# Kernel tuning notes

Hardware: AMD Instinct MI355X
Metric: run time of the kernel (lower is better)

The kernel has to match this reference:

```python
import jax, jax.numpy as jnp
import numpy as np

B, L, FUT = 500, 100, 4  # dialogs, utterances per dialog, to_future_link
N = B * L
IN, HID, NC = 1024, 512, 7


def _build_graph():
    # per-dialog local edges: node i -> i (self) and i -> i+1..i+FUT (within dialog)
    i = np.arange(L)[:, None]                       # [L,1]
    off = np.arange(FUT + 1)[None, :]               # [1,FUT+1]
    tgt_local = i + off                             # [L,FUT+1]
    valid = tgt_local < L
    src_local = np.broadcast_to(i, tgt_local.shape)[valid]
    tgt_local = tgt_local[valid]                    # [E_per]
    base = (np.arange(B) * L)[:, None]              # [B,1]
    src = (base + src_local[None, :]).reshape(-1)
    tgt = (base + tgt_local[None, :]).reshape(-1)
    edges = np.stack([src, tgt], axis=0).astype(np.int64)  # [2,E], E=245000
    rng = np.random.RandomState(0)
    speakers = rng.randint(0, 2, size=N).astype(np.int64)
    rel = (speakers[src] * speakers[tgt]).astype(np.int64)  # in {0,1}
    return edges, rel


def setup_inputs() -> dict:
    key = jax.random.key(0)
    ks = jax.random.split(key, 8)
    edges, rel = _build_graph()
    s = 0.02
    return {
        "x": jax.random.normal(ks[0], (N, IN), dtype=jnp.float32),
        "edges": jnp.asarray(edges),
        "relation_type": jnp.asarray(rel),
        "w_rel": jax.random.normal(ks[1], (2, IN, HID), dtype=jnp.float32) * s,
        "w_root": jax.random.normal(ks[2], (IN, HID), dtype=jnp.float32) * s,
        "b_rgcn": jnp.zeros((HID,), jnp.float32),
        "w_gc_rel": jax.random.normal(ks[3], (HID, HID), dtype=jnp.float32) * s,
        "w_gc_root": jax.random.normal(ks[4], (HID, HID), dtype=jnp.float32) * s,
        "b_gc": jnp.zeros((HID,), jnp.float32),
        "w_skip": jax.random.normal(ks[5], (IN, HID), dtype=jnp.float32) * s,
        "b_skip": jnp.zeros((HID,), jnp.float32),
        "w_clf": jax.random.normal(ks[6], (HID, NC), dtype=jnp.float32) * s,
        "b_clf": jnp.zeros((NC,), jnp.float32),
    }


def reference(x, edges, relation_type, w_rel, w_root, b_rgcn,
              w_gc_rel, w_gc_root, b_gc, w_skip, b_skip, w_clf, b_clf):
    n = x.shape[0]
    src, tgt = edges[0], edges[1]
    # --- RGCNConv(IN, HID, 2), aggr='mean' per relation, root weight + bias ---
    x_src = x[src]  # [E, IN] gather
    h = x @ w_root + b_rgcn
    for r in range(2):
        m = (relation_type == r).astype(x.dtype)                    # [E]
        s = jax.ops.segment_sum(x_src * m[:, None], tgt, num_segments=n)  # [N,IN]
        c = jax.ops.segment_sum(m, tgt, num_segments=n)             # [N]
        mean = s / jnp.maximum(c, 1.0)[:, None]                     # scatter-mean, 0 if empty
        h = h + mean @ w_rel[r]
    # --- GraphConv(HID, HID), aggr='add': W_rel * sum_j x_j + W_root * x_i + b ---
    agg = jax.ops.segment_sum(h[src], tgt, num_segments=n)          # [N,HID]
    h2 = agg @ w_gc_rel + b_gc + h @ w_gc_root
    # --- classify(h2 + skip(x)) ---
    out = (h2 + x @ w_skip + b_skip) @ w_clf + b_clf                # [N,NC]
    return out
```

## Files before the change

### kernel.cpp

```cpp
#include <hip/hip_runtime.h>


#define DIAG_L 100
#define EPERD  490
#define NC     7
#define NROWS  50000
#define NBLK   782

using u16 = unsigned short;
using u32 = unsigned int;
typedef __bf16 bf16x8 __attribute__((ext_vector_type(8)));
typedef float  f32x4  __attribute__((ext_vector_type(4)));

__device__ __forceinline__ u16 f2b(float f) {
  u32 u = __builtin_bit_cast(u32, f);
  u32 r = (u + 0x7FFFu + ((u >> 16) & 1u)) >> 16;
  return (u16)r;
}
__device__ __forceinline__ u32 pk2(float a, float b) {
  return (u32)f2b(a) | ((u32)f2b(b) << 16);
}

__device__ __forceinline__ int pre_edges(int s) {
  int d = s - 96;
  return 5 * s - (d > 0 ? ((d * (d + 1)) >> 1) : 0);
}

__global__ __launch_bounds__(64)
void k_t1n(const float* __restrict__ w_gc_root, const float* __restrict__ w_gc_rel,
           const float* __restrict__ w_clf, const float* __restrict__ b_gc,
           const float* __restrict__ b_skip, const float* __restrict__ b_clf,
           float* __restrict__ tbl, float* __restrict__ cvec) {
  const int bid = blockIdx.x, l = threadIdx.x;
  if (bid < 1024) {
    const int which = bid & 1, k = bid >> 1;
    const float* src = (which ? w_gc_rel : w_gc_root) + (size_t)k * 512;
    float p[7] = {0.f, 0.f, 0.f, 0.f, 0.f, 0.f, 0.f};
#pragma unroll
    for (int jj = 0; jj < 8; ++jj) {
      int j = jj * 64 + l;
      float sv = src[j];
      const float* wc = w_clf + (size_t)j * 7;
#pragma unroll
      for (int c = 0; c < 7; ++c) p[c] += sv * wc[c];
    }
#pragma unroll
    for (int c = 0; c < 7; ++c)
      for (int d = 32; d; d >>= 1) p[c] += __shfl_xor(p[c], d);
    if (l == 0) {
      float* tr = tbl + which * 4096 + k * 8;
#pragma unroll
      for (int c = 0; c < 7; ++c) tr[c] = p[c];
      tr[7] = 0.f;
    }
  } else {
    const int c = bid - 1024;
    float s = 0.f;
#pragma unroll
    for (int jj = 0; jj < 8; ++jj) {
      int j = jj * 64 + l;
      s += (b_gc[j] + b_skip[j]) * w_clf[(size_t)j * 7 + c];
    }
    for (int d = 32; d; d >>= 1) s += __shfl_xor(s, d);
    if (l == 0) cvec[16 + c] = s + b_clf[c];
  }
}

__global__ __launch_bounds__(256)
void k_w64n(const float* __restrict__ w_root, const float* __restrict__ w_rel,
            const float* __restrict__ w_skip, const float* __restrict__ w_clf,
            const float* __restrict__ b_rgcn, const float* __restrict__ tbl,
            u16* __restrict__ BT, float* __restrict__ cvec) {
  const int bid = blockIdx.x;
  if (bid < 1024) {
    const int k = bid, tid = threadIdx.x;
    const int n = tid >> 2, jq = tid & 3, g = n >> 3, c = n & 7;
    float p = 0.f;
    if (g < 7 && c < 7) {
      const float* src;
      switch (g % 3) {
        case 0: src = w_root; break;
        case 1: src = w_rel; break;
        default: src = w_rel + 524288; break;
      }
      if (g == 6) src = w_skip;
      src += (size_t)k * 512;
      if (g == 6) {
#pragma unroll 4
        for (int i = 0; i < 128; ++i) {
          int j = jq * 128 + i;
          p += src[j] * w_clf[(size_t)j * 7 + c];
        }
      } else {
        const float* T = tbl + (g >= 3 ? 4096 : 0);
#pragma unroll 4
        for (int i = 0; i < 128; ++i) {
          int j = jq * 128 + i;
          p += src[j] * T[j * 8 + c];
        }
      }
    }
    p += __shfl_xor(p, 1); p += __shfl_xor(p, 2);
    if (jq == 0) BT[(size_t)n * 1024 + k] = f2b(p);
  } else {
    const int idx = bid - 1024;
    const int l = threadIdx.x;
    if (l < 64) {
      const float* T = tbl + (idx >= 8 ? 4096 : 0);
      const int cc = idx & 7;
      float s = 0.f;
#pragma unroll
      for (int jj = 0; jj < 8; ++jj) {
        int j = jj * 64 + l;
        s += b_rgcn[j] * T[j * 8 + cc];
      }
      for (int d = 32; d; d >>= 1) s += __shfl_xor(s, d);
      if (l == 0) cvec[idx] = s;
    }
  }
}

__device__ __forceinline__ void gload16(const void* g, void* l) {
  __builtin_amdgcn_global_load_lds(
      (const __attribute__((address_space(1))) u32*)g,
      (__attribute__((address_space(3))) u32*)l, 16, 0, 0);
}

__global__ __launch_bounds__(256, 5)
void k_px3(const float* __restrict__ x, const u16* __restrict__ BT,
           float* __restrict__ P) {
  __shared__ char lds[32768];
  const int tid = threadIdx.x;
  const int w = tid >> 6, l = tid & 63;
  const int rl = l & 15, sl = l >> 4;
  const int rb = blockIdx.x << 6;
  const int sx = (rl & 7) << 4;

  const int ar = tid >> 2, ac4 = tid & 3;
  int arow = rb + ar; if (arow > NROWS - 1) arow = NROWS - 1;
  const char* axp = (const char*)x + (size_t)arow * 4096 + ac4 * 64;
  const int aw0 = ar * 128 + ((ac4 * 32) ^ ((ar & 7) << 4));
  const int aw1 = ar * 128 + ((ac4 * 32 + 16) ^ ((ar & 7) << 4));

  const char* bsrc[2]; int blbase[2];
#pragma unroll
  for (int is = 0; is < 2; ++is) {
    int ci = is * 256 + tid;
    int r = ci >> 3, g = ci & 7, gp = g ^ (r & 7);
    bsrc[is] = (const char*)BT + (size_t)r * 2048 + gp * 16;
    blbase[is] = __builtin_amdgcn_readfirstlane(16384 + is * 4096 + w * 1024);
  }

  float4 av[4];
#define ALOAD(kt) { av[0] = *(const float4*)(axp + (kt) * 256);      \
                    av[1] = *(const float4*)(axp + (kt) * 256 + 16); \
                    av[2] = *(const float4*)(axp + (kt) * 256 + 32); \
                    av[3] = *(const float4*)(axp + (kt) * 256 + 48); }
#define AWRITE(bf) { uint4 q0, q1;                                   \
    q0.x = pk2(av[0].x, av[0].y); q0.y = pk2(av[0].z, av[0].w);      \
    q0.z = pk2(av[1].x, av[1].y); q0.w = pk2(av[1].z, av[1].w);      \
    q1.x = pk2(av[2].x, av[2].y); q1.y = pk2(av[2].z, av[2].w);      \
    q1.z = pk2(av[3].x, av[3].y); q1.w = pk2(av[3].z, av[3].w);      \
    *(uint4*)(lds + (bf) * 8192 + aw0) = q0;                         \
    *(uint4*)(lds + (bf) * 8192 + aw1) = q1; }
#define BSTAGE(bf, kt) {                                             \
    gload16(bsrc[0] + (kt) * 128, lds + blbase[0] + (bf) * 8192);    \
    gload16(bsrc[1] + (kt) * 128, lds + blbase[1] + (bf) * 8192); }

  f32x4 acc[4];
#pragma unroll
  for (int nf = 0; nf < 4; ++nf) acc[nf] = f32x4{0.f, 0.f, 0.f, 0.f};

  ALOAD(0); BSTAGE(0, 0); AWRITE(0);
  ALOAD(1); BSTAGE(1, 1); AWRITE(1);
  asm volatile("s_waitcnt lgkmcnt(0)" ::: "memory");
  __builtin_amdgcn_s_barrier();

  for (int t = 0; t < 16; ++t) {
    const int b = t & 1;
    const char* Ab = lds + b * 8192 + (w * 16 + rl) * 128;
    const char* Bb = lds + 16384 + b * 8192 + rl * 128;
    const int kn = (t + 2 < 16) ? t + 2 : 15;
    ALOAD(kn);
#pragma unroll
    for (int ks = 0; ks < 2; ++ks) {
      const int ko = (ks * 64 + sl * 16) ^ sx;
      bf16x8 af = *(const bf16x8*)(Ab + ko);
      bf16x8 b0 = *(const bf16x8*)(Bb + ko);
      bf16x8 b1 = *(const bf16x8*)(Bb + 2048 + ko);
      bf16x8 b2 = *(const bf16x8*)(Bb + 4096 + ko);
      bf16x8 b3 = *(const bf16x8*)(Bb + 6144 + ko);
      acc[0] = __builtin_amdgcn_mfma_f32_16x16x32_bf16(af, b0, acc[0], 0, 0, 0);
      acc[1] = __builtin_amdgcn_mfma_f32_16x16x32_bf16(af, b1, acc[1], 0, 0, 0);
      acc[2] = __builtin_amdgcn_mfma_f32_16x16x32_bf16(af, b2, acc[2], 0, 0, 0);
      acc[3] = __builtin_amdgcn_mfma_f32_16x16x32_bf16(af, b3, acc[3], 0, 0, 0);
    }
    __builtin_amdgcn_s_barrier();
    BSTAGE(b, kn);
    AWRITE(b);
    asm volatile("s_waitcnt lgkmcnt(0)" ::: "memory");
    __builtin_amdgcn_s_barrier();
  }
  asm volatile("s_waitcnt vmcnt(0)" ::: "memory");
#undef ALOAD
#undef AWRITE
#undef BSTAGE

  const int pr = rb + w * 16 + sl * 4;
#pragma unroll
  for (int nf = 0; nf < 4; ++nf)
#pragma unroll
    for (int j = 0; j < 4; ++j)
      P[(size_t)(pr + j) * 64 + nf * 16 + rl] = acc[nf][j];
}

__global__ __launch_bounds__(128)
void k_out(const float* __restrict__ P, const int* __restrict__ rel,
           const float* __restrict__ cvec, float* __restrict__ out) {
  __shared__ float pt[64 * 100 + 16 * 100];
  float* hb = pt + 6400;
  const int d = blockIdx.x;
  const int tid = threadIdx.x;
  const float* Pd = P + (size_t)d * DIAG_L * 64;

  for (int it = tid; it < 6400; it += 128) {
    int r = it >> 6, c = it & 63;
    pt[c * 100 + r] = Pd[it];
  }
  __syncthreads();

  const int ebase = d * EPERD;
  if (tid < DIAG_L) {
    const int u = tid;
    const int slo = (u > 4) ? u - 4 : 0;
    float S0A[7], S1A[7], S0B[7], S1B[7];
#pragma unroll
    for (int c = 0; c < 7; ++c) { S0A[c] = 0.f; S1A[c] = 0.f; S0B[c] = 0.f; S1B[c] = 0.f; }
    float c0 = 0.f, c1 = 0.f;
    for (int s = slo; s <= u; ++s) {
      int r = rel[ebase + pre_edges(s) + (u - s)];
      float m0 = r ? 0.f : 1.f, m1 = 1.f - m0;
      c0 += m0; c1 += m1;
#pragma unroll
      for (int c = 0; c < 7; ++c) {
        S0A[c] += m0 * pt[(8 + c)  * 100 + s];
        S1A[c] += m1 * pt[(16 + c) * 100 + s];
        S0B[c] += m0 * pt[(32 + c) * 100 + s];
        S1B[c] += m1 * pt[(40 + c) * 100 + s];
      }
    }
    float inv0 = 1.f / fmaxf(c0, 1.f), inv1 = 1.f / fmaxf(c1, 1.f);
#pragma unroll
    for (int c = 0; c < 7; ++c) {
      hb[c * 100 + u]       = pt[c * 100 + u]        + cvec[c]     + inv0 * S0A[c] + inv1 * S1A[c];
      hb[(8 + c) * 100 + u] = pt[(24 + c) * 100 + u] + cvec[8 + c] + inv0 * S0B[c] + inv1 * S1B[c];
    }
  }
  __syncthreads();

  if (tid < DIAG_L) {
    const int t = tid;
    const int slo = (t > 4) ? t - 4 : 0;
    float o[7];
#pragma unroll
    for (int c = 0; c < 7; ++c)
      o[c] = hb[c * 100 + t] + pt[(48 + c) * 100 + t] + cvec[16 + c];
    for (int s = slo; s <= t; ++s) {
#pragma unroll
      for (int c = 0; c < 7; ++c) o[c] += hb[(8 + c) * 100 + s];
    }
    float* op = out + ((size_t)d * DIAG_L + t) * NC;
#pragma unroll
    for (int c = 0; c < 7; ++c) op[c] = o[c];
  }
}

extern "C" void kernel_launch(void* const* d_in, const int* in_sizes, int n_in,
                              void* d_out, int out_size, void* d_ws, size_t ws_size,
                              hipStream_t stream) {
  const float* x         = (const float*)d_in[0];
  const int*   rel       = (const int*)d_in[2];
  const float* w_rel     = (const float*)d_in[3];
  const float* w_root    = (const float*)d_in[4];
  const float* b_rgcn    = (const float*)d_in[5];
  const float* w_gc_rel  = (const float*)d_in[6];
  const float* w_gc_root = (const float*)d_in[7];
  const float* b_gc      = (const float*)d_in[8];
  const float* w_skip    = (const float*)d_in[9];
  const float* b_skip    = (const float*)d_in[10];
  const float* w_clf     = (const float*)d_in[11];
  const float* b_clf     = (const float*)d_in[12];
  float* out = (float*)d_out;

  char* ws = (char*)d_ws;
  float* P    = (float*)(ws);
  u16*   BT   = (u16*)(ws + 12845056);
  float* tbl  = (float*)(ws + 12976128);
  float* cvec = (float*)(ws + 13008896);

  k_t1n<<<1031, 64, 0, stream>>>(w_gc_root, w_gc_rel, w_clf, b_gc, b_skip, b_clf, tbl, cvec);
  k_w64n<<<1040, 256, 0, stream>>>(w_root, w_rel, w_skip, w_clf, b_rgcn, tbl, BT, cvec);
  k_px3<<<NBLK, 256, 0, stream>>>(x, BT, P);
  k_out<<<500, 128, 0, stream>>>(P, rel, cvec, out);
}
```

Baseline: 82.12 us.

## Fuse projection GEMM with graph aggregation and classifier output using halo rows

Merges the bf16 MFMA projection kernel and the per-dialog aggregation/output kernel into one kernel. Each workgroup now computes 80 projected rows: its own 64 plus a 16-row halo of earlier rows, with wave 0 doing the extra MFMA tile. The results stay in LDS, and the RGCN mean, GraphConv sum and output are computed there directly, removing the global write and re-read of the intermediate P buffer and one kernel launch. It also remaps block IDs in an XCD-aware way. In exchange it recomputes the halo rows, loads wave 0 more heavily than the others, and enlarges LDS, lowering the occupancy target from 5 to 4.

Result: slower. 84.06 us (+2.4%).

```diff
diff --git a/kernel.cpp b/kernel.cpp
--- a/kernel.cpp
+++ b/kernel.cpp
@@ -126,50 +126,83 @@
       (__attribute__((address_space(3))) u32*)l, 16, 0, 0);
 }
 
-__global__ __launch_bounds__(256, 5)
-void k_px3(const float* __restrict__ x, const u16* __restrict__ BT,
-           float* __restrict__ P) {
-  __shared__ char lds[32768];
+__global__ __launch_bounds__(256, 4)
+void k_pxo(const float* __restrict__ x, const u16* __restrict__ BT,
+           const int* __restrict__ rel, const float* __restrict__ cvec,
+           float* __restrict__ out, int nwg) {
+  __shared__ char lds[36864];
   const int tid = threadIdx.x;
   const int w = tid >> 6, l = tid & 63;
   const int rl = l & 15, sl = l >> 4;
-  const int rb = blockIdx.x << 6;
   const int sx = (rl & 7) << 4;
 
-  const int ar = tid >> 2, ac4 = tid & 3;
-  int arow = rb + ar; if (arow > NROWS - 1) arow = NROWS - 1;
-  const char* axp = (const char*)x + (size_t)arow * 4096 + ac4 * 64;
-  const int aw0 = ar * 128 + ((ac4 * 32) ^ ((ar & 7) << 4));
-  const int aw1 = ar * 128 + ((ac4 * 32 + 16) ^ ((ar & 7) << 4));
+  const int bid = blockIdx.x;
+  const int q = nwg >> 3, r8 = nwg & 7;
+  const int xcd = bid & 7, bix = bid >> 3;
+  const int wg = (xcd < r8 ? xcd * (q + 1) : r8 * (q + 1) + (xcd - r8) * q) + bix;
+  const int gbase = wg * 64 - 16;
+
+  const bool dual = (tid < 64);
+  const int r0c = tid >> 2, s0c = tid & 3;
+  int g0r = gbase + r0c;
+  g0r = g0r < 0 ? 0 : (g0r > NROWS - 1 ? NROWS - 1 : g0r);
+  const char* axp0 = (const char*)x + (size_t)g0r * 4096 + s0c * 64;
+  const int a00 = r0c * 128 + ((s0c * 32) ^ ((r0c & 7) << 4));
+  const int a01 = r0c * 128 + ((s0c * 32 + 16) ^ ((r0c & 7) << 4));
+  const int r1c = 64 + (tid >> 2);
+  int g1r = gbase + r1c;
+  g1r = g1r < 0 ? 0 : (g1r > NROWS - 1 ? NROWS - 1 : g1r);
+  const char* axp1 = (const char*)x + (size_t)g1r * 4096 + s0c * 64;
+  const int a10 = r1c * 128 + ((s0c * 32) ^ ((r1c & 7) << 4));
+  const int a11 = r1c * 128 + ((s0c * 32 + 16) ^ ((r1c & 7) << 4));
 
   const char* bsrc[2]; int blbase[2];
 #pragma unroll
   for (int is = 0; is < 2; ++is) {
     int ci = is * 256 + tid;
-    int r = ci >> 3, g = ci & 7, gp = g ^ (r & 7);
-    bsrc[is] = (const char*)BT + (size_t)r * 2048 + gp * 16;
-    blbase[is] = __builtin_amdgcn_readfirstlane(16384 + is * 4096 + w * 1024);
-  }
-
-  float4 av[4];
-#define ALOAD(kt) { av[0] = *(const float4*)(axp + (kt) * 256);      \
-                    av[1] = *(const float4*)(axp + (kt) * 256 + 16); \
-                    av[2] = *(const float4*)(axp + (kt) * 256 + 32); \
-                    av[3] = *(const float4*)(axp + (kt) * 256 + 48); }
-#define AWRITE(bf) { uint4 q0, q1;                                   \
-    q0.x = pk2(av[0].x, av[0].y); q0.y = pk2(av[0].z, av[0].w);      \
-    q0.z = pk2(av[1].x, av[1].y); q0.w = pk2(av[1].z, av[1].w);      \
-    q1.x = pk2(av[2].x, av[2].y); q1.y = pk2(av[2].z, av[2].w);      \
-    q1.z = pk2(av[3].x, av[3].y); q1.w = pk2(av[3].z, av[3].w);      \
-    *(uint4*)(lds + (bf) * 8192 + aw0) = q0;                         \
-    *(uint4*)(lds + (bf) * 8192 + aw1) = q1; }
-#define BSTAGE(bf, kt) {                                             \
-    gload16(bsrc[0] + (kt) * 128, lds + blbase[0] + (bf) * 8192);    \
+    int rB = ci >> 3, gB = ci & 7, gp = gB ^ (rB & 7);
+    bsrc[is] = (const char*)BT + (size_t)rB * 2048 + gp * 16;
+    blbase[is] = __builtin_amdgcn_readfirstlane(20480 + is * 4096 + w * 1024);
+  }
+
+  float4 av0[4], av1[4];
+
+#define ALOAD(kt) { \
+    av0[0] = *(const float4*)(axp0 + (kt) * 256);        \
+    av0[1] = *(const float4*)(axp0 + (kt) * 256 + 16);   \
+    av0[2] = *(const float4*)(axp0 + (kt) * 256 + 32);   \
+    av0[3] = *(const float4*)(axp0 + (kt) * 256 + 48);   \
+    if (dual) {                                          \
+      av1[0] = *(const float4*)(axp1 + (kt) * 256);      \
+      av1[1] = *(const float4*)(axp1 + (kt) * 256 + 16); \
+      av1[2] = *(const float4*)(axp1 + (kt) * 256 + 32); \
+      av1[3] = *(const float4*)(axp1 + (kt) * 256 + 48); \
+    } }
+#define AWRITE(bf) { uint4 q0, q1;                              \
+    q0.x = pk2(av0[0].x, av0[0].y); q0.y = pk2(av0[0].z, av0[0].w); \
+    q0.z = pk2(av0[1].x, av0[1].y); q0.w = pk2(av0[1].z, av0[1].w); \
+    q1.x = pk2(av0[2].x, av0[2].y); q1.y = pk2(av0[2].z, av0[2].w); \
+    q1.z = pk2(av0[3].x, av0[3].y); q1.w = pk2(av0[3].z, av0[3].w); \
+    *(uint4*)(lds + (bf) * 10240 + a00) = q0;                   \
+    *(uint4*)(lds + (bf) * 10240 + a01) = q1;                   \
+    if (dual) { uint4 q2, q3;                                   \
+      q2.x = pk2(av1[0].x, av1[0].y); q2.y = pk2(av1[0].z, av1[0].w); \
+      q2.z = pk2(av1[1].x, av1[1].y); q2.w = pk2(av1[1].z, av1[1].w); \
+      q3.x = pk2(av1[2].x, av1[2].y); q3.y = pk2(av1[2].z, av1[2].w); \
+      q3.z = pk2(av1[3].x, av1[3].y); q3.w = pk2(av1[3].z, av1[3].w); \
+      *(uint4*)(lds + (bf) * 10240 + a10) = q2;                 \
+      *(uint4*)(lds + (bf) * 10240 + a11) = q3;                 \
+    } }
+#define BSTAGE(bf, kt) {                                            \
+    gload16(bsrc[0] + (kt) * 128, lds + blbase[0] + (bf) * 8192);   \
     gload16(bsrc[1] + (kt) * 128, lds + blbase[1] + (bf) * 8192); }
 
-  f32x4 acc[4];
-#pragma unroll
-  for (int nf = 0; nf < 4; ++nf) acc[nf] = f32x4{0.f, 0.f, 0.f, 0.f};
+  f32x4 acc[4], acc4[4];
+#pragma unroll
+  for (int nf = 0; nf < 4; ++nf) {
+    acc[nf]  = f32x4{0.f, 0.f, 0.f, 0.f};
+    acc4[nf] = f32x4{0.f, 0.f, 0.f, 0.f};
+  }
 
   ALOAD(0); BSTAGE(0, 0); AWRITE(0);
   ALOAD(1); BSTAGE(1, 1); AWRITE(1);
@@ -178,10 +211,11 @@
 
   for (int t = 0; t < 16; ++t) {
     const int b = t & 1;
-    const char* Ab = lds + b * 8192 + (w * 16 + rl) * 128;
-    const char* Bb = lds + 16384 + b * 8192 + rl * 128;
     const int kn = (t + 2 < 16) ? t + 2 : 15;
     ALOAD(kn);
+    const char* Ab  = lds + b * 10240 + (w * 16 + rl) * 128;
+    const char* Ab4 = lds + b * 10240 + (64 + rl) * 128;
+    const char* Bb  = lds + 20480 + b * 8192 + rl * 128;
 #pragma unroll
     for (int ks = 0; ks < 2; ++ks) {
       const int ko = (ks * 64 + sl * 16) ^ sx;
@@ -194,6 +228,13 @@
       acc[1] = __builtin_amdgcn_mfma_f32_16x16x32_bf16(af, b1, acc[1], 0, 0, 0);
       acc[2] = __builtin_amdgcn_mfma_f32_16x16x32_bf16(af, b2, acc[2], 0, 0, 0);
       acc[3] = __builtin_amdgcn_mfma_f32_16x16x32_bf16(af, b3, acc[3], 0, 0, 0);
+      if (w == 0) {
+        bf16x8 af4 = *(const bf16x8*)(Ab4 + ko);
+        acc4[0] = __builtin_amdgcn_mfma_f32_16x16x32_bf16(af4, b0, acc4[0], 0, 0, 0);
+        acc4[1] = __builtin_amdgcn_mfma_f32_16x16x32_bf16(af4, b1, acc4[1], 0, 0, 0);
+        acc4[2] = __builtin_amdgcn_mfma_f32_16x16x32_bf16(af4, b2, acc4[2], 0, 0, 0);
+        acc4[3] = __builtin_amdgcn_mfma_f32_16x16x32_bf16(af4, b3, acc4[3], 0, 0, 0);
+      }
     }
     __builtin_amdgcn_s_barrier();
     BSTAGE(b, kn);
@@ -201,77 +242,83 @@
     asm volatile("s_waitcnt lgkmcnt(0)" ::: "memory");
     __builtin_amdgcn_s_barrier();
   }
-  asm volatile("s_waitcnt vmcnt(0)" ::: "memory");
+  asm volatile("s_waitcnt vmcnt(0) lgkmcnt(0)" ::: "memory");
+  __syncthreads();
 #undef ALOAD
 #undef AWRITE
 #undef BSTAGE
 
-  const int pr = rb + w * 16 + sl * 4;
-#pragma unroll
-  for (int nf = 0; nf < 4; ++nf)
-#pragma unroll
-    for (int j = 0; j < 4; ++j)
-      P[(size_t)(pr + j) * 64 + nf * 16 + rl] = acc[nf][j];
-}
-
-__global__ __launch_bounds__(128)
-void k_out(const float* __restrict__ P, const int* __restrict__ rel,
-           const float* __restrict__ cvec, float* __restrict__ out) {
-  __shared__ float pt[64 * 100 + 16 * 100];
-  float* hb = pt + 6400;
-  const int d = blockIdx.x;
-  const int tid = threadIdx.x;
-  const float* Pd = P + (size_t)d * DIAG_L * 64;
-
-  for (int it = tid; it < 6400; it += 128) {
-    int r = it >> 6, c = it & 63;
-    pt[c * 100 + r] = Pd[it];
+  float* pt  = (float*)lds;
+  float* hbf = (float*)(lds + 21440);
+  {
+    const int rb0 = w * 16 + sl * 4;
+#pragma unroll
+    for (int nf = 0; nf < 4; ++nf)
+#pragma unroll
+      for (int j = 0; j < 4; ++j)
+        pt[(rb0 + j) * 67 + nf * 16 + rl] = acc[nf][j];
+    if (w == 0) {
+      const int rb4 = 64 + sl * 4;
+#pragma unroll
+      for (int nf = 0; nf < 4; ++nf)
+#pragma unroll
+        for (int j = 0; j < 4; ++j)
+          pt[(rb4 + j) * 67 + nf * 16 + rl] = acc4[nf][j];
+    }
   }
   __syncthreads();
 
-  const int ebase = d * EPERD;
-  if (tid < DIAG_L) {
-    const int u = tid;
-    const int slo = (u > 4) ? u - 4 : 0;
-    float S0A[7], S1A[7], S0B[7], S1B[7];
-#pragma unroll
-    for (int c = 0; c < 7; ++c) { S0A[c] = 0.f; S1A[c] = 0.f; S0B[c] = 0.f; S1B[c] = 0.f; }
-    float c0 = 0.f, c1 = 0.f;
-    for (int s = slo; s <= u; ++s) {
-      int r = rel[ebase + pre_edges(s) + (u - s)];
-      float m0 = r ? 0.f : 1.f, m1 = 1.f - m0;
-      c0 += m0; c1 += m1;
+  if (tid >= 8 && tid < 80) {
+    const int i = tid, g = gbase + i;
+    if (g >= 0 && g < NROWS) {
+      const int d = g / DIAG_L, dstart = d * DIAG_L;
+      const int slo = (g - 4 > dstart) ? g - 4 : dstart;
+      float S0A[7], S1A[7], S0B[7], S1B[7];
+#pragma unroll
+      for (int c = 0; c < 7; ++c) { S0A[c] = 0.f; S1A[c] = 0.f; S0B[c] = 0.f; S1B[c] = 0.f; }
+      float c0 = 0.f, c1 = 0.f;
+      for (int s = slo; s <= g; ++s) {
+        int rr = rel[d * EPERD + pre_edges(s - dstart) + (g - s)];
+        float m0 = rr ? 0.f : 1.f, m1 = 1.f - m0;
+        c0 += m0; c1 += m1;
+        const float* pr = pt + (s - gbase) * 67;
+#pragma unroll
+        for (int c = 0; c < 7; ++c) {
+          S0A[c] += m0 * pr[8 + c];
+          S1A[c] += m1 * pr[16 + c];
+          S0B[c] += m0 * pr[32 + c];
+          S1B[c] += m1 * pr[40 + c];
+        }
+      }
+      float inv0 = 1.f / fmaxf(c0, 1.f), inv1 = 1.f / fmaxf(c1, 1.f);
+      const float* pi = pt + i * 67;
 #pragma unroll
       for (int c = 0; c < 7; ++c) {
-        S0A[c] += m0 * pt[(8 + c)  * 100 + s];
-        S1A[c] += m1 * pt[(16 + c) * 100 + s];
-        S0B[c] += m0 * pt[(32 + c) * 100 + s];
-        S1B[c] += m1 * pt[(40 + c) * 100 + s];
-      }
-    }
-    float inv0 = 1.f / fmaxf(c0, 1.f), inv1 = 1.f / fmaxf(c1, 1.f);
-#pragma unroll
-    for (int c = 0; c < 7; ++c) {
-      hb[c * 100 + u]       = pt[c * 100 + u]        + cvec[c]     + inv0 * S0A[c] + inv1 * S1A[c];
-      hb[(8 + c) * 100 + u] = pt[(24 + c) * 100 + u] + cvec[8 + c] + inv0 * S0B[c] + inv1 * S1B[c];
+        hbf[i * 16 + c]     = pi[c]      + cvec[c]     + inv0 * S0A[c] + inv1 * S1A[c];
+        hbf[i * 16 + 8 + c] = pi[24 + c] + cvec[8 + c] + inv0 * S0B[c] + inv1 * S1B[c];
+      }
     }
   }
   __syncthreads();
 
-  if (tid < DIAG_L) {
-    const int t = tid;
-    const int slo = (t > 4) ? t - 4 : 0;
-    float o[7];
-#pragma unroll
-    for (int c = 0; c < 7; ++c)
-      o[c] = hb[c * 100 + t] + pt[(48 + c) * 100 + t] + cvec[16 + c];
-    for (int s = slo; s <= t; ++s) {
-#pragma unroll
-      for (int c = 0; c < 7; ++c) o[c] += hb[(8 + c) * 100 + s];
-    }
-    float* op = out + ((size_t)d * DIAG_L + t) * NC;
-#pragma unroll
-    for (int c = 0; c < 7; ++c) op[c] = o[c];
+  if (tid >= 16 && tid < 80) {
+    const int i = tid, g = gbase + i;
+    if (g < NROWS) {
+      const int d = g / DIAG_L, dstart = d * DIAG_L;
+      const int slo = (g - 4 > dstart) ? g - 4 : dstart;
+      float o[7];
+#pragma unroll
+      for (int c = 0; c < 7; ++c)
+        o[c] = hbf[i * 16 + c] + pt[i * 67 + 48 + c] + cvec[16 + c];
+      for (int s = slo; s <= g; ++s) {
+        const float* hs = hbf + (s - gbase) * 16 + 8;
+#pragma unroll
+        for (int c = 0; c < 7; ++c) o[c] += hs[c];
+      }
+      float* op = out + (size_t)g * NC;
+#pragma unroll
+      for (int c = 0; c < 7; ++c) op[c] = o[c];
+    }
   }
 }
 
@@ -293,13 +340,11 @@
   float* out = (float*)d_out;
 
   char* ws = (char*)d_ws;
-  float* P    = (float*)(ws);
-  u16*   BT   = (u16*)(ws + 12845056);
-  float* tbl  = (float*)(ws + 12976128);
-  float* cvec = (float*)(ws + 13008896);
+  u16*   BT   = (u16*)(ws);
+  float* tbl  = (float*)(ws + 131072);
+  float* cvec = (float*)(ws + 163840);
 
   k_t1n<<<1031, 64, 0, stream>>>(w_gc_root, w_gc_rel, w_clf, b_gc, b_skip, b_clf, tbl, cvec);
   k_w64n<<<1040, 256, 0, stream>>>(w_root, w_rel, w_skip, w_clf, b_rgcn, tbl, BT, cvec);
-  k_px3<<<NBLK, 256, 0, stream>>>(x, BT, P);
-  k_out<<<500, 128, 0, stream>>>(P, rel, cvec, out);
-}
+  k_pxo<<<NBLK, 256, 0, stream>>>(x, BT, rel, cvec, out, NBLK);
+}
```

## Replace LDS-staged GEMM with per-wave register-fed MFMA loading directly from global

Applied to the files above, without the earlier changes.

The projection kernel no longer stages x and the packed weights through shared memory with barriers. Each wave now loads its own 16 rows of x straight into registers, converts them to bf16 in registers, and reads B fragments directly from global memory (L2-cached), double-buffering two 1024-byte K chunks in registers. This removes the LDS traffic and block-wide barriers, and it drops the occupancy hint. The cost is much higher register pressure (32 float4 buffers) and uncoalesced, repeated global reads of B across waves.

Result: slower. 128.7 us (+56.7%).

```diff
diff --git a/kernel.cpp b/kernel.cpp
--- a/kernel.cpp
+++ b/kernel.cpp
@@ -120,93 +120,58 @@
   }
 }
 
-__device__ __forceinline__ void gload16(const void* g, void* l) {
-  __builtin_amdgcn_global_load_lds(
-      (const __attribute__((address_space(1))) u32*)g,
-      (__attribute__((address_space(3))) u32*)l, 16, 0, 0);
-}
-
-__global__ __launch_bounds__(256, 5)
-void k_px3(const float* __restrict__ x, const u16* __restrict__ BT,
+__global__ __launch_bounds__(256)
+void k_px5(const float* __restrict__ x, const u16* __restrict__ BT,
            float* __restrict__ P) {
-  __shared__ char lds[32768];
-  const int tid = threadIdx.x;
-  const int w = tid >> 6, l = tid & 63;
+  const int w = threadIdx.x >> 6, l = threadIdx.x & 63;
   const int rl = l & 15, sl = l >> 4;
-  const int rb = blockIdx.x << 6;
-  const int sx = (rl & 7) << 4;
-
-  const int ar = tid >> 2, ac4 = tid & 3;
-  int arow = rb + ar; if (arow > NROWS - 1) arow = NROWS - 1;
-  const char* axp = (const char*)x + (size_t)arow * 4096 + ac4 * 64;
-  const int aw0 = ar * 128 + ((ac4 * 32) ^ ((ar & 7) << 4));
-  const int aw1 = ar * 128 + ((ac4 * 32 + 16) ^ ((ar & 7) << 4));
-
-  const char* bsrc[2]; int blbase[2];
-#pragma unroll
-  for (int is = 0; is < 2; ++is) {
-    int ci = is * 256 + tid;
-    int r = ci >> 3, g = ci & 7, gp = g ^ (r & 7);
-    bsrc[is] = (const char*)BT + (size_t)r * 2048 + gp * 16;
-    blbase[is] = __builtin_amdgcn_readfirstlane(16384 + is * 4096 + w * 1024);
-  }
-
-  float4 av[4];
-#define ALOAD(kt) { av[0] = *(const float4*)(axp + (kt) * 256);      \
-                    av[1] = *(const float4*)(axp + (kt) * 256 + 16); \
-                    av[2] = *(const float4*)(axp + (kt) * 256 + 32); \
-                    av[3] = *(const float4*)(axp + (kt) * 256 + 48); }
-#define AWRITE(bf) { uint4 q0, q1;                                   \
-    q0.x = pk2(av[0].x, av[0].y); q0.y = pk2(av[0].z, av[0].w);      \
-    q0.z = pk2(av[1].x, av[1].y); q0.w = pk2(av[1].z, av[1].w);      \
-    q1.x = pk2(av[2].x, av[2].y); q1.y = pk2(av[2].z, av[2].w);      \
-    q1.z = pk2(av[3].x, av[3].y); q1.w = pk2(av[3].z, av[3].w);      \
-    *(uint4*)(lds + (bf) * 8192 + aw0) = q0;                         \
-    *(uint4*)(lds + (bf) * 8192 + aw1) = q1; }
-#define BSTAGE(bf, kt) {                                             \
-    gload16(bsrc[0] + (kt) * 128, lds + blbase[0] + (bf) * 8192);    \
-    gload16(bsrc[1] + (kt) * 128, lds + blbase[1] + (bf) * 8192); }
+  const int rb = (blockIdx.x * 4 + w) << 4;
+  int row = rb + rl; if (row > NROWS - 1) row = NROWS - 1;
+  const char* xr = (const char*)x + (size_t)row * 4096 + sl * 32;
+  const char* bp = (const char*)BT + rl * 2048 + sl * 16;
+
+  float4 avA[16], avB[16];
+
+#define ALOADM(p, m) { _Pragma("unroll")                         \
+    for (int j = 0; j < 8; ++j) {                                \
+      p[2 * j]     = *(const float4*)(xr + (m) * 1024 + j * 128);      \
+      p[2 * j + 1] = *(const float4*)(xr + (m) * 1024 + j * 128 + 16); \
+    } }
+#define COMPM(p, m) { _Pragma("unroll")                          \
+    for (int j = 0; j < 8; ++j) {                                \
+      uint4 ap;                                                  \
+      ap.x = pk2(p[2 * j].x,     p[2 * j].y);                    \
+      ap.y = pk2(p[2 * j].z,     p[2 * j].w);                    \
+      ap.z = pk2(p[2 * j + 1].x, p[2 * j + 1].y);                \
+      ap.w = pk2(p[2 * j + 1].z, p[2 * j + 1].w);                \
+      bf16x8 af = __builtin_bit_cast(bf16x8, ap);                \
+      const int ks = (m) * 8 + j;                                \
+      bf16x8 b0 = *(const bf16x8*)(bp + ks * 64);                \
+      bf16x8 b1 = *(const bf16x8*)(bp + 32768 + ks * 64);        \
+      bf16x8 b2 = *(const bf16x8*)(bp + 65536 + ks * 64);        \
+      bf16x8 b3 = *(const bf16x8*)(bp + 98304 + ks * 64);        \
+      acc[0] = __builtin_amdgcn_mfma_f32_16x16x32_bf16(af, b0, acc[0], 0, 0, 0); \
+      acc[1] = __builtin_amdgcn_mfma_f32_16x16x32_bf16(af, b1, acc[1], 0, 0, 0); \
+      acc[2] = __builtin_amdgcn_mfma_f32_16x16x32_bf16(af, b2, acc[2], 0, 0, 0); \
+      acc[3] = __builtin_amdgcn_mfma_f32_16x16x32_bf16(af, b3, acc[3], 0, 0, 0); \
+    } }
 
   f32x4 acc[4];
 #pragma unroll
   for (int nf = 0; nf < 4; ++nf) acc[nf] = f32x4{0.f, 0.f, 0.f, 0.f};
 
-  ALOAD(0); BSTAGE(0, 0); AWRITE(0);
-  ALOAD(1); BSTAGE(1, 1); AWRITE(1);
-  asm volatile("s_waitcnt lgkmcnt(0)" ::: "memory");
-  __builtin_amdgcn_s_barrier();
-
-  for (int t = 0; t < 16; ++t) {
-    const int b = t & 1;
-    const char* Ab = lds + b * 8192 + (w * 16 + rl) * 128;
-    const char* Bb = lds + 16384 + b * 8192 + rl * 128;
-    const int kn = (t + 2 < 16) ? t + 2 : 15;
-    ALOAD(kn);
-#pragma unroll
-    for (int ks = 0; ks < 2; ++ks) {
-      const int ko = (ks * 64 + sl * 16) ^ sx;
-      bf16x8 af = *(const bf16x8*)(Ab + ko);
-      bf16x8 b0 = *(const bf16x8*)(Bb + ko);
-      bf16x8 b1 = *(const bf16x8*)(Bb + 2048 + ko);
-      bf16x8 b2 = *(const bf16x8*)(Bb + 4096 + ko);
-      bf16x8 b3 = *(const bf16x8*)(Bb + 6144 + ko);
-      acc[0] = __builtin_amdgcn_mfma_f32_16x16x32_bf16(af, b0, acc[0], 0, 0, 0);
-      acc[1] = __builtin_amdgcn_mfma_f32_16x16x32_bf16(af, b1, acc[1], 0, 0, 0);
-      acc[2] = __builtin_amdgcn_mfma_f32_16x16x32_bf16(af, b2, acc[2], 0, 0, 0);
-      acc[3] = __builtin_amdgcn_mfma_f32_16x16x32_bf16(af, b3, acc[3], 0, 0, 0);
-    }
-    __builtin_amdgcn_s_barrier();
-    BSTAGE(b, kn);
-    AWRITE(b);
-    asm volatile("s_waitcnt lgkmcnt(0)" ::: "memory");
-    __builtin_amdgcn_s_barrier();
-  }
-  asm volatile("s_waitcnt vmcnt(0)" ::: "memory");
-#undef ALOAD
-#undef AWRITE
-#undef BSTAGE
-
-  const int pr = rb + w * 16 + sl * 4;
+  ALOADM(avA, 0);
+  ALOADM(avB, 1);
+  COMPM(avA, 0);
+  ALOADM(avA, 2);
+  COMPM(avB, 1);
+  ALOADM(avB, 3);
+  COMPM(avA, 2);
+  COMPM(avB, 3);
+#undef ALOADM
+#undef COMPM
+
+  const int pr = rb + sl * 4;
 #pragma unroll
   for (int nf = 0; nf < 4; ++nf)
 #pragma unroll
@@ -300,6 +265,6 @@
 
   k_t1n<<<1031, 64, 0, stream>>>(w_gc_root, w_gc_rel, w_clf, b_gc, b_skip, b_clf, tbl, cvec);
   k_w64n<<<1040, 256, 0, stream>>>(w_root, w_rel, w_skip, w_clf, b_rgcn, tbl, BT, cvec);
-  k_px3<<<NBLK, 256, 0, stream>>>(x, BT, P);
+  k_px5<<<NBLK, 256, 0, stream>>>(x, BT, P);
   k_out<<<500, 128, 0, stream>>>(P, rel, cvec, out);
 }
```
